# Performance work log

Measured on AMD Instinct MI355X. Metric: run time of the kernel, lower is better.

The kernel has to match this reference:

```python
import jax, jax.numpy as jnp
import numpy as np

EPS = 1e-6
NEG_SLOPE = 0.2

B, C_IN, N, K = 4, 64, 40960, 16
C_OUT = 64


def setup_inputs() -> dict:
    key = jax.random.key(0)
    k1, k2, k3 = jax.random.split(key, 3)
    feature = jax.random.normal(k1, (B, C_IN, N, 1), dtype=jnp.float32)
    neigh_idx = jax.random.randint(k2, (B, N, K), 0, N, dtype=jnp.int64)
    # 1x1 conv kernel [C_out, C_in] (kaiming-like scale), no bias since bn=True
    W = jax.random.normal(k3, (C_OUT, C_IN), dtype=jnp.float32) * np.float32(np.sqrt(2.0 / C_IN))
    gamma = jnp.ones((C_OUT,), dtype=jnp.float32)
    beta = jnp.zeros((C_OUT,), dtype=jnp.float32)
    return {"feature": feature, "W": W, "gamma": gamma, "beta": beta, "neigh_idx": neigh_idx}


def _gather_neighbour(pc, neigh_idx):
    # pc: [B, C, N]; neigh_idx: [B, N, K] -> [B, C, N, K]
    return jax.vmap(lambda p, idx: p[:, idx])(pc, neigh_idx)


def reference(feature, W, gamma, beta, neigh_idx):
    pc = feature[..., 0]                       # [B, C, N]
    f_neigh = _gather_neighbour(pc, neigh_idx) # [B, C, N, K]
    x = jnp.concatenate([feature, f_neigh], axis=-1)  # [B, C, N, K+1]
    # 1x1 conv (no bias)
    y = jnp.einsum('oc,bcnk->bonk', W, x)      # [B, C_out, N, K+1]
    # BatchNorm2d (training mode: batch stats over B,N,K+1), eps=1e-6
    mean = jnp.mean(y, axis=(0, 2, 3), keepdims=True)
    var = jnp.mean(jnp.square(y - mean), axis=(0, 2, 3), keepdims=True)
    yn = (y - mean) * jax.lax.rsqrt(var + EPS)
    yn = yn * gamma[None, :, None, None] + beta[None, :, None, None]
    # LeakyReLU(0.2)
    act = jnp.where(yn >= 0, yn, NEG_SLOPE * yn)
    # sum over neighbor axis, keepdim
    return jnp.sum(act, axis=-1, keepdims=True)  # [B, C_out, N, 1]
```

## Files before the change

### kernel.cpp

```cpp
#include <hip/hip_runtime.h>
#include <hip/hip_fp16.h>

typedef _Float16 h2 __attribute__((ext_vector_type(2)));

#define BB 4
#define CIN 64
#define COUT 64
#define NN 40960
#define KK 16
#define GBLK (BB * NN / 256)
#define FPAD 264
#define WPAD 68
#define HP 32
#define HR 2
#define HBINS (NN / HR)
#define HWORDS (HBINS / 2)

__global__ __launch_bounds__(256) void k_hist(const int* __restrict__ idx,
                                              unsigned int* __restrict__ hist) {
    __shared__ unsigned int bins[HWORDS];
    const int tid = threadIdx.x;
    const int b = blockIdx.x >> 6;
    const int p = (blockIdx.x >> 1) & (HP - 1);
    const int r = blockIdx.x & (HR - 1);
    const int lo = r * HBINS;

#pragma unroll
    for (int i = 0; i < HWORDS / 256; ++i) bins[i * 256 + tid] = 0u;
    __syncthreads();

    const int SHARE = NN * KK / HP;
    const int4* src = (const int4*)(idx + (size_t)b * NN * KK + (size_t)p * SHARE);
#pragma unroll 4
    for (int i = 0; i < SHARE / 4 / 256; ++i) {
        int4 v = src[i * 256 + tid];
        unsigned a0 = (unsigned)(v.x - lo), a1 = (unsigned)(v.y - lo);
        unsigned a2 = (unsigned)(v.z - lo), a3 = (unsigned)(v.w - lo);
        if (a0 < HBINS) atomicAdd(&bins[a0 >> 1], 1u << ((a0 & 1) * 16));
        if (a1 < HBINS) atomicAdd(&bins[a1 >> 1], 1u << ((a1 & 1) * 16));
        if (a2 < HBINS) atomicAdd(&bins[a2 >> 1], 1u << ((a2 & 1) * 16));
        if (a3 < HBINS) atomicAdd(&bins[a3 >> 1], 1u << ((a3 & 1) * 16));
    }
    __syncthreads();
    unsigned int* dst = hist + (size_t)blockIdx.x * HWORDS;
#pragma unroll
    for (int i = 0; i < HWORDS / 256; ++i) dst[i * 256 + tid] = bins[i * 256 + tid];
}

__global__ __launch_bounds__(256) void k_gemm(const float* __restrict__ feat,
                                              const float* __restrict__ W,
                                              const unsigned int* __restrict__ hist,
                                              __half* __restrict__ g,
                                              float* __restrict__ partials) {
    __shared__ float Wt_s[64 * WPAD];
    __shared__ float feat_s[16 * FPAD];
    __shared__ float w_s[256];

    const int tid = threadIdx.x;
    const int b   = blockIdx.x / (NN / 256);
    const int n0  = (blockIdx.x % (NN / 256)) * 256;

    {
        const int n  = n0 + tid;
        const int r  = n / HBINS;
        const int ml = n - r * HBINS;
        const int w  = ml >> 1;
        const int sh = (ml & 1) * 16;
        unsigned s = 1u;
#pragma unroll
        for (int p = 0; p < HP; ++p)
            s += (hist[(size_t)((b * HP + p) * HR + r) * HWORDS + w] >> sh) & 0xffffu;
        w_s[tid] = (float)s;
    }

#pragma unroll
    for (int it = 0; it < 16; ++it) {
        int c = tid & 63;
        int o = it * 4 + (tid >> 6);
        Wt_s[c * WPAD + o] = W[o * 64 + c];
    }

    const int to = tid & 7;
    const int tn = tid >> 3;

    float acc[8][8];
#pragma unroll
    for (int i = 0; i < 8; ++i)
#pragma unroll
        for (int j = 0; j < 8; ++j) acc[i][j] = 0.f;

    const float* fb = feat + (size_t)b * CIN * NN + n0;

    for (int cc0 = 0; cc0 < 64; cc0 += 16) {
        __syncthreads();
        {
            int row = tid >> 4;
            int col = (tid & 15) * 4;
            const float* src = fb + (size_t)(cc0 + row) * NN + col;
#pragma unroll
            for (int q = 0; q < 4; ++q) {
                float4 v = *(const float4*)(src + q * 64);
                *(float4*)&feat_s[row * FPAD + col + q * 64] = v;
            }
        }
        __syncthreads();

#pragma unroll
        for (int cc = 0; cc < 16; ++cc) {
            int c = cc0 + cc;
            float4 w0 = *(const float4*)&Wt_s[c * WPAD + to * 8];
            float4 w1 = *(const float4*)&Wt_s[c * WPAD + to * 8 + 4];
            float4 f0 = *(const float4*)&feat_s[cc * FPAD + tn * 8];
            float4 f1 = *(const float4*)&feat_s[cc * FPAD + tn * 8 + 4];
            float wv[8] = {w0.x, w0.y, w0.z, w0.w, w1.x, w1.y, w1.z, w1.w};
            float fv[8] = {f0.x, f0.y, f0.z, f0.w, f1.x, f1.y, f1.z, f1.w};
#pragma unroll
            for (int i = 0; i < 8; ++i)
#pragma unroll
                for (int j = 0; j < 8; ++j)
                    acc[i][j] = fmaf(wv[i], fv[j], acc[i][j]);
        }
    }

    __half* gb = g + ((size_t)b * NN + n0) * 64;
#pragma unroll
    for (int j = 0; j < 8; ++j) {
        int n = tn * 8 + j;
        union { uint4 u; h2 h[4]; } P;
#pragma unroll
        for (int h = 0; h < 4; ++h) {
            h2 t;
            t.x = (_Float16)acc[2 * h][j];
            t.y = (_Float16)acc[2 * h + 1][j];
            P.h[h] = t;
        }
        *(uint4*)&gb[(size_t)n * 64 + to * 8] = P.u;
    }

    float wgt[8];
#pragma unroll
    for (int j = 0; j < 8; ++j) wgt[j] = w_s[tn * 8 + j];
    float s1[8], s2[8];
#pragma unroll
    for (int i = 0; i < 8; ++i) { s1[i] = 0.f; s2[i] = 0.f; }
#pragma unroll
    for (int j = 0; j < 8; ++j)
#pragma unroll
        for (int i = 0; i < 8; ++i) {
            float wv = wgt[j] * acc[i][j];
            s1[i] += wv;
            s2[i] += wv * acc[i][j];
        }

    __syncthreads();
    float* red = feat_s;
#pragma unroll
    for (int i = 0; i < 8; ++i) {
        int o = to * 8 + i;
        red[o * 33 + tn]        = s1[i];
        red[2112 + o * 33 + tn] = s2[i];
    }
    __syncthreads();
    if (tid < 128) {
        int arr = tid >> 6, o = tid & 63;
        const float* base = red + arr * 2112 + o * 33;
        float s = 0.f;
#pragma unroll
        for (int t = 0; t < 32; ++t) s += base[t];
        partials[blockIdx.x * 128 + arr * 64 + o] = s;
    }
}

__global__ __launch_bounds__(1024) void k_finalize(const float* __restrict__ partials,
                                                   const float* __restrict__ gamma,
                                                   const float* __restrict__ beta,
                                                   _Float16* __restrict__ params_h) {
    const int i = threadIdx.x & 127;
    const int r = threadIdx.x >> 7;
    double a0 = 0, a1 = 0, a2 = 0, a3 = 0;
    for (int base = r; base < GBLK; base += 32) {
        a0 += (double)partials[(base)      * 128 + i];
        a1 += (double)partials[(base + 8)  * 128 + i];
        a2 += (double)partials[(base + 16) * 128 + i];
        a3 += (double)partials[(base + 24) * 128 + i];
    }
    __shared__ double red[8][128];
    red[r][i] = (a0 + a1) + (a2 + a3);
    __syncthreads();
    if (threadIdx.x < 64) {
        const int o = threadIdx.x;
        double s1 = 0.0, s2 = 0.0;
#pragma unroll
        for (int rr = 0; rr < 8; ++rr) { s1 += red[rr][o]; s2 += red[rr][64 + o]; }
        const double TOT = (double)BB * NN * (KK + 1);
        double mean = s1 / TOT;
        double var  = s2 / TOT - mean * mean;
        double inv  = 1.0 / sqrt(var + 1e-6);
        float scale = (float)inv * gamma[o];
        float shift = beta[o] - (float)mean * scale;
        params_h[o]      = (_Float16)scale;
        params_h[64 + o] = (_Float16)shift;
    }
}

__global__ __launch_bounds__(256) void k_final(const __half* __restrict__ g,
                                               const int* __restrict__ idx,
                                               const _Float16* __restrict__ params_h,
                                               float* __restrict__ out) {
    const int tid  = threadIdx.x;
    const int lane = tid & 63;
    const int wave = tid >> 6;
    const int b     = (blockIdx.x & 7) >> 1;
    const int chunk = ((blockIdx.x >> 3) << 1) | (blockIdx.x & 1);
    const int n0    = chunk * 64;

    __shared__ int   idx_s[64 * 17];
    __shared__ float tile[64 * 65];

    {
        const int4* src = (const int4*)(idx + ((size_t)b * NN + n0) * KK);
        int4 v = src[tid];
        int row = tid >> 2, col = (tid & 3) * 4;
        idx_s[row * 17 + col + 0] = v.x;
        idx_s[row * 17 + col + 1] = v.y;
        idx_s[row * 17 + col + 2] = v.z;
        idx_s[row * 17 + col + 3] = v.w;
    }

    const int r  = lane >> 3;
    const int q8 = (lane & 7) * 8;
    h2 sc2[4], sh2[4];
#pragma unroll
    for (int h = 0; h < 4; ++h) {
        h2 a, s;
        a.x = params_h[q8 + 2 * h];     a.y = params_h[q8 + 2 * h + 1];
        s.x = params_h[64 + q8 + 2 * h]; s.y = params_h[64 + q8 + 2 * h + 1];
        sc2[h] = a; sh2[h] = s;
    }
    __syncthreads();

    const __half* gb = g + (size_t)b * NN * 64;

#pragma unroll
    for (int rr = 0; rr < 2; ++rr) {
        const int nl = wave * 16 + rr * 8 + r;
        h2 acc[4];
#pragma unroll
        for (int h = 0; h < 4; ++h) acc[h] = (h2)(_Float16)0;

#pragma unroll
        for (int k = -1; k < KK; ++k) {
            int m = (k < 0) ? (n0 + nl) : idx_s[nl * 17 + k];
            union { uint4 u; h2 h[4]; } U;
            U.u = *(const uint4*)(gb + (size_t)m * 64 + q8);
#pragma unroll
            for (int h = 0; h < 4; ++h) {
                h2 t = U.h[h] * sc2[h] + sh2[h];
                acc[h] += __builtin_elementwise_max(t, t * (_Float16)0.2f);
            }
        }
        float* tr = &tile[nl * 65 + q8];
#pragma unroll
        for (int h = 0; h < 4; ++h) {
            tr[2 * h]     = (float)acc[h].x;
            tr[2 * h + 1] = (float)acc[h].y;
        }
    }
    __syncthreads();
    const int j   = tid & 63;
    const int sub = tid >> 6;
#pragma unroll
    for (int ob = 0; ob < 16; ++ob) {
        int o = ob * 4 + sub;
        out[(size_t)(b * 64 + o) * NN + n0 + j] = tile[j * 65 + o];
    }
}

extern "C" void kernel_launch(void* const* d_in, const int* in_sizes, int n_in,
                              void* d_out, int out_size, void* d_ws, size_t ws_size,
                              hipStream_t stream) {
    const float* feat  = (const float*)d_in[0];
    const float* W     = (const float*)d_in[1];
    const float* gamma = (const float*)d_in[2];
    const float* beta  = (const float*)d_in[3];
    const int*   idx   = (const int*)d_in[4];
    float* out = (float*)d_out;

    char* ws = (char*)d_ws;
    __half* g = (__half*)ws;
    size_t off = (size_t)BB * NN * 64 * sizeof(__half);
    unsigned int* hist = (unsigned int*)(ws + off);
    off += (size_t)BB * HP * HR * HWORDS * sizeof(unsigned int);
    float* partials = (float*)(ws + off);
    off += (size_t)GBLK * 128 * sizeof(float);
    _Float16* params_h = (_Float16*)(ws + off);

    k_hist<<<BB * HP * HR, 256, 0, stream>>>(idx, hist);
    k_gemm<<<GBLK, 256, 0, stream>>>(feat, W, hist, g, partials);
    k_finalize<<<1, 1024, 0, stream>>>(partials, gamma, beta, params_h);
    k_final<<<(BB * NN) / 64, 256, 0, stream>>>(g, idx, params_h, out);
}
```

Baseline: 157.9 us.

## Drop finalize kernel via atomic stats and pack histogram bins to 8-bit

Replaces per-block partials plus a single-block finalize kernel with float atomicAdd into 128 global sums, zeroed by the histogram kernel. Each final-stage block computes the BN scale and shift itself. Histogram bins are packed four per word, halving LDS and histogram memory, and block indices are remapped across batches. This risks count overflow above 255 and nondeterministic, lower-precision fp32 statistics.

```diff
diff --git a/kernel.cpp b/kernel.cpp
--- a/kernel.cpp
+++ b/kernel.cpp
@@ -14,16 +14,19 @@
 #define HP 32
 #define HR 2
 #define HBINS (NN / HR)
-#define HWORDS (HBINS / 2)
+#define HWORDS (HBINS / 4)
 
 __global__ __launch_bounds__(256) void k_hist(const int* __restrict__ idx,
-                                              unsigned int* __restrict__ hist) {
+                                              unsigned int* __restrict__ hist,
+                                              float* __restrict__ sums) {
     __shared__ unsigned int bins[HWORDS];
     const int tid = threadIdx.x;
-    const int b = blockIdx.x >> 6;
-    const int p = (blockIdx.x >> 1) & (HP - 1);
-    const int r = blockIdx.x & (HR - 1);
+    const int p = blockIdx.x >> 3;
+    const int b = (blockIdx.x & 7) >> 1;
+    const int r = blockIdx.x & 1;
     const int lo = r * HBINS;
+
+    if (blockIdx.x == 0 && tid < 128) sums[tid] = 0.f;
 
 #pragma unroll
     for (int i = 0; i < HWORDS / 256; ++i) bins[i * 256 + tid] = 0u;
@@ -36,13 +39,13 @@
         int4 v = src[i * 256 + tid];
         unsigned a0 = (unsigned)(v.x - lo), a1 = (unsigned)(v.y - lo);
         unsigned a2 = (unsigned)(v.z - lo), a3 = (unsigned)(v.w - lo);
-        if (a0 < HBINS) atomicAdd(&bins[a0 >> 1], 1u << ((a0 & 1) * 16));
-        if (a1 < HBINS) atomicAdd(&bins[a1 >> 1], 1u << ((a1 & 1) * 16));
-        if (a2 < HBINS) atomicAdd(&bins[a2 >> 1], 1u << ((a2 & 1) * 16));
-        if (a3 < HBINS) atomicAdd(&bins[a3 >> 1], 1u << ((a3 & 1) * 16));
-    }
-    __syncthreads();
-    unsigned int* dst = hist + (size_t)blockIdx.x * HWORDS;
+        if (a0 < HBINS) atomicAdd(&bins[a0 >> 2], 1u << ((a0 & 3) * 8));
+        if (a1 < HBINS) atomicAdd(&bins[a1 >> 2], 1u << ((a1 & 3) * 8));
+        if (a2 < HBINS) atomicAdd(&bins[a2 >> 2], 1u << ((a2 & 3) * 8));
+        if (a3 < HBINS) atomicAdd(&bins[a3 >> 2], 1u << ((a3 & 3) * 8));
+    }
+    __syncthreads();
+    unsigned int* dst = hist + (size_t)((b * HP + p) * HR + r) * HWORDS;
 #pragma unroll
     for (int i = 0; i < HWORDS / 256; ++i) dst[i * 256 + tid] = bins[i * 256 + tid];
 }
@@ -51,25 +54,26 @@
                                               const float* __restrict__ W,
                                               const unsigned int* __restrict__ hist,
                                               __half* __restrict__ g,
-                                              float* __restrict__ partials) {
+                                              float* __restrict__ sums) {
     __shared__ float Wt_s[64 * WPAD];
     __shared__ float feat_s[16 * FPAD];
     __shared__ float w_s[256];
 
-    const int tid = threadIdx.x;
-    const int b   = blockIdx.x / (NN / 256);
-    const int n0  = (blockIdx.x % (NN / 256)) * 256;
+    const int tid   = threadIdx.x;
+    const int b     = (blockIdx.x & 7) >> 1;
+    const int chunk = (blockIdx.x & 1) * 80 + (blockIdx.x >> 3);
+    const int n0    = chunk * 256;
 
     {
         const int n  = n0 + tid;
         const int r  = n / HBINS;
         const int ml = n - r * HBINS;
-        const int w  = ml >> 1;
-        const int sh = (ml & 1) * 16;
+        const int w  = ml >> 2;
+        const int sh = (ml & 3) * 8;
         unsigned s = 1u;
 #pragma unroll
         for (int p = 0; p < HP; ++p)
-            s += (hist[(size_t)((b * HP + p) * HR + r) * HWORDS + w] >> sh) & 0xffffu;
+            s += (hist[(size_t)((b * HP + p) * HR + r) * HWORDS + w] >> sh) & 0xffu;
         w_s[tid] = (float)s;
     }
 
@@ -167,45 +171,15 @@
         float s = 0.f;
 #pragma unroll
         for (int t = 0; t < 32; ++t) s += base[t];
-        partials[blockIdx.x * 128 + arr * 64 + o] = s;
-    }
-}
-
-__global__ __launch_bounds__(1024) void k_finalize(const float* __restrict__ partials,
-                                                   const float* __restrict__ gamma,
-                                                   const float* __restrict__ beta,
-                                                   _Float16* __restrict__ params_h) {
-    const int i = threadIdx.x & 127;
-    const int r = threadIdx.x >> 7;
-    double a0 = 0, a1 = 0, a2 = 0, a3 = 0;
-    for (int base = r; base < GBLK; base += 32) {
-        a0 += (double)partials[(base)      * 128 + i];
-        a1 += (double)partials[(base + 8)  * 128 + i];
-        a2 += (double)partials[(base + 16) * 128 + i];
-        a3 += (double)partials[(base + 24) * 128 + i];
-    }
-    __shared__ double red[8][128];
-    red[r][i] = (a0 + a1) + (a2 + a3);
-    __syncthreads();
-    if (threadIdx.x < 64) {
-        const int o = threadIdx.x;
-        double s1 = 0.0, s2 = 0.0;
-#pragma unroll
-        for (int rr = 0; rr < 8; ++rr) { s1 += red[rr][o]; s2 += red[rr][64 + o]; }
-        const double TOT = (double)BB * NN * (KK + 1);
-        double mean = s1 / TOT;
-        double var  = s2 / TOT - mean * mean;
-        double inv  = 1.0 / sqrt(var + 1e-6);
-        float scale = (float)inv * gamma[o];
-        float shift = beta[o] - (float)mean * scale;
-        params_h[o]      = (_Float16)scale;
-        params_h[64 + o] = (_Float16)shift;
+        atomicAdd(&sums[arr * 64 + o], s);
     }
 }
 
 __global__ __launch_bounds__(256) void k_final(const __half* __restrict__ g,
                                                const int* __restrict__ idx,
-                                               const _Float16* __restrict__ params_h,
+                                               const float* __restrict__ sums,
+                                               const float* __restrict__ gamma,
+                                               const float* __restrict__ beta,
                                                float* __restrict__ out) {
     const int tid  = threadIdx.x;
     const int lane = tid & 63;
@@ -216,6 +190,7 @@
 
     __shared__ int   idx_s[64 * 17];
     __shared__ float tile[64 * 65];
+    __shared__ float prm[128];
 
     {
         const int4* src = (const int4*)(idx + ((size_t)b * NN + n0) * KK);
@@ -227,17 +202,28 @@
         idx_s[row * 17 + col + 3] = v.w;
     }
 
+    if (tid < 64) {
+        const double TOT = (double)BB * NN * (KK + 1);
+        double mean = (double)sums[tid] / TOT;
+        double var  = (double)sums[64 + tid] / TOT - mean * mean;
+        double inv  = 1.0 / sqrt(var + 1e-6);
+        float scale = (float)inv * gamma[tid];
+        float shift = beta[tid] - (float)mean * scale;
+        prm[tid]      = scale;
+        prm[64 + tid] = shift;
+    }
+    __syncthreads();
+
     const int r  = lane >> 3;
     const int q8 = (lane & 7) * 8;
     h2 sc2[4], sh2[4];
 #pragma unroll
     for (int h = 0; h < 4; ++h) {
         h2 a, s;
-        a.x = params_h[q8 + 2 * h];     a.y = params_h[q8 + 2 * h + 1];
-        s.x = params_h[64 + q8 + 2 * h]; s.y = params_h[64 + q8 + 2 * h + 1];
+        a.x = (_Float16)prm[q8 + 2 * h];      a.y = (_Float16)prm[q8 + 2 * h + 1];
+        s.x = (_Float16)prm[64 + q8 + 2 * h]; s.y = (_Float16)prm[64 + q8 + 2 * h + 1];
         sc2[h] = a; sh2[h] = s;
     }
-    __syncthreads();
 
     const __half* gb = g + (size_t)b * NN * 64;
 
@@ -291,12 +277,9 @@
     size_t off = (size_t)BB * NN * 64 * sizeof(__half);
     unsigned int* hist = (unsigned int*)(ws + off);
     off += (size_t)BB * HP * HR * HWORDS * sizeof(unsigned int);
-    float* partials = (float*)(ws + off);
-    off += (size_t)GBLK * 128 * sizeof(float);
-    _Float16* params_h = (_Float16*)(ws + off);
-
-    k_hist<<<BB * HP * HR, 256, 0, stream>>>(idx, hist);
-    k_gemm<<<GBLK, 256, 0, stream>>>(feat, W, hist, g, partials);
-    k_finalize<<<1, 1024, 0, stream>>>(partials, gamma, beta, params_h);
-    k_final<<<(BB * NN) / 64, 256, 0, stream>>>(g, idx, params_h, out);
-}
+    float* sums = (float*)(ws + off);
+
+    k_hist<<<BB * HP * HR, 256, 0, stream>>>(idx, hist, sums);
+    k_gemm<<<GBLK, 256, 0, stream>>>(feat, W, hist, g, sums);
+    k_final<<<(BB * NN) / 64, 256, 0, stream>>>(g, idx, sums, gamma, beta, out);
+}
```

After: 155.3 us. No clear change (-1.7%).
